# Kernel tuning notes

Measured on AMD Instinct MI355X. Metric: run time of the kernel, lower is better.

## Reference

```python
import jax, jax.numpy as jnp
import numpy as np

N, K, CIN, HID, COUT, E, MH = 8192, 200, 512, 256, 40, 5, 64
KG = K // E
EPS = 1e-5


def setup_inputs() -> dict:
    key = jax.random.key(0)
    ks = jax.random.split(key, 20)
    inp = {
        "X": jax.random.normal(ks[0], (N, CIN), jnp.float32),
        "La": jax.random.uniform(ks[1], (K,), jnp.float32),
        "U": jax.random.normal(ks[2], (N, K), jnp.float32),
        # 5 EigenExperts, each mlp = Linear(1,64) -> ReLU -> Linear(64,64) -> ReLU -> Linear(64,1)
        "eW1": jax.random.normal(ks[3], (E, MH), jnp.float32) * 0.5,
        "eb1": jax.random.normal(ks[4], (E, MH), jnp.float32) * 0.1,
        "eW2": jax.random.normal(ks[5], (E, MH, MH), jnp.float32) * (1.0 / np.sqrt(MH)),
        "eb2": jax.random.normal(ks[6], (E, MH), jnp.float32) * 0.1,
        "eW3": jax.random.normal(ks[7], (E, MH), jnp.float32) * (1.0 / np.sqrt(MH)),
        "eb3": jax.random.normal(ks[8], (E,), jnp.float32) * 0.1,
        # gate: Linear(5,5) -> ReLU -> Linear(5,5) -> Softmax
        "gW1": jax.random.normal(ks[9], (E, E), jnp.float32) * 0.4,
        "gb1": jax.random.normal(ks[10], (E,), jnp.float32) * 0.1,
        "gW2": jax.random.normal(ks[11], (E, E), jnp.float32) * 0.4,
        "gb2": jax.random.normal(ks[12], (E,), jnp.float32) * 0.1,
        # W: Linear(in_channels, hidden_dim)
        "Ww": jax.random.normal(ks[13], (CIN, HID), jnp.float32) * (1.0 / np.sqrt(CIN)),
        "Wb": jax.random.normal(ks[14], (HID,), jnp.float32) * 0.1,
        # BatchNorm1d(hidden_dim), training-mode batch stats
        "bn_gamma": jnp.ones((HID,), jnp.float32),
        "bn_beta": jnp.zeros((HID,), jnp.float32),
        # MLP: Linear(hidden_dim, out_channels)
        "Mw": jax.random.normal(ks[15], (HID, COUT), jnp.float32) * (1.0 / np.sqrt(HID)),
        "Mb": jax.random.normal(ks[16], (COUT,), jnp.float32) * 0.1,
    }
    return inp


def reference(X, La, U, eW1, eb1, eW2, eb2, eW3, eb3, gW1, gb1, gW2, gb2, Ww, Wb, bn_gamma, bn_beta, Mw, Mb):
    n, k = U.shape
    e = eW1.shape[0]
    kg = k // e
    # group eigenvector columns: U[:, i*kg:(i+1)*kg] for expert i -> [n, e, kg]
    Ue = U.reshape(n, e, kg)
    # EigenExpert tiny MLP applied elementwise over entries of each column, then mean over nodes
    h1 = jax.nn.relu(jnp.einsum('nek,eh->nekh', Ue, eW1) + eb1[None, :, None, :])
    h2 = jax.nn.relu(jnp.einsum('nekh,ehg->nekg', h1, eW2) + eb2[None, :, None, :])
    v = jnp.einsum('nekh,eh->nek', h2, eW3) + eb3[None, :, None]
    V = v.mean(axis=0)                      # [e, kg] importance per eigenvector
    # gate on per-group mean eigenvalue
    stats = La.reshape(e, kg).mean(axis=1)  # [e]
    g = jax.nn.relu(stats @ gW1 + gb1) @ gW2 + gb2
    g = jax.nn.softmax(g, axis=-1)          # [e]
    # sum_i g_i * U_i diag(V_i) U_i^T == (U * s) @ U^T with per-column scale s
    s = (g[:, None] * V).reshape(k)         # [k]
    A = (U * s[None, :]) @ U.T              # [n, n]
    out = A @ X                             # [n, cin]
    hidden = out @ Ww + Wb                  # [n, hid]
    mu = hidden.mean(axis=0)
    var = hidden.var(axis=0)                # biased, as torch BN uses for normalization
    h = (hidden - mu) * jax.lax.rsqrt(var + EPS) * bn_gamma + bn_beta
    h = jax.nn.relu(h)                      # dropout is identity (eval)
    logits = h @ Mw + Mb
    return jax.nn.log_softmax(logits, axis=1), hidden
```

## Files before the change

kernel.cpp:

```cpp
#include <hip/hip_runtime.h>
#include <hip/hip_bf16.h>

#define N_    8192
#define K_    200
#define CIN_  512
#define HID_  256
#define COUT_ 40
#define E_    5
#define MH_   64
#define KG_   40
#define EPS_  1e-5f

#define WS_VSUM  0
#define WS_BNSUM 256
#define WS_T     768
#define WS_S     103168
#define WS_G     103424

#define KSPLIT_ 16

typedef __bf16 bf16x8 __attribute__((ext_vector_type(8)));
typedef float  f32x16 __attribute__((ext_vector_type(16)));

__device__ __forceinline__ uint packbf(float a, float b) {
    union { __bf16 h[2]; uint u; } p;
    p.h[0] = (__bf16)a; p.h[1] = (__bf16)b;
    return p.u;
}

union UB { uint4 q; bf16x8 v; };

__global__ __launch_bounds__(256) void k_expert(
    const float* __restrict__ U,
    const float* __restrict__ eW1, const float* __restrict__ eb1,
    const float* __restrict__ eW2, const float* __restrict__ eb2,
    const float* __restrict__ eW3, const float* __restrict__ eb3,
    float* __restrict__ Vsum)
{
    const int e   = blockIdx.x;
    const int tid = threadIdx.x;
    const int w   = tid >> 6;
    const int l   = tid & 63;
    const int lo  = l & 31;
    const int hi  = l >> 5;

    __shared__ uint  spk[4][8][64][4];
    __shared__ float sW1[MH_], sb1[MH_], sb2s[MH_], sW3s[MH_];
    __shared__ float colsum[KG_];

    if (tid < MH_) {
        sW1[tid]  = eW1[e*MH_ + tid];
        sb1[tid]  = eb1[e*MH_ + tid];
        sb2s[tid] = eb2[e*MH_ + tid];
        sW3s[tid] = eW3[e*MH_ + tid];
    }
    if (tid < KG_) colsum[tid] = 0.f;
    const float b3 = eb3[e];

    bf16x8 fa[2][4];
    {
        const float* W2e = eW2 + e*MH_*MH_;
        #pragma unroll
        for (int mt = 0; mt < 2; ++mt) {
            const int grow = mt*32 + lo;
            #pragma unroll
            for (int t = 0; t < 4; ++t) {
                const int k0 = 16*t + 8*hi;
                union { uint u[4]; bf16x8 v; } fb;
                #pragma unroll
                for (int r = 0; r < 4; ++r) {
                    const float x0 = W2e[(k0+2*r  )*MH_ + grow];
                    const float x1 = W2e[(k0+2*r+1)*MH_ + grow];
                    fb.u[r] = packbf(x0, x1);
                }
                fa[mt][t] = fb.v;
            }
        }
    }
    __syncthreads();

    for (int it = 0; it < 4; ++it) {
        const int tile  = (blockIdx.y*16 + it*4 + w);
        const int elem0 = tile * 64;
        const int idx   = elem0 + l;
        const int n     = idx / KG_;
        const int kg    = idx - n*KG_;
        const float u   = U[n*K_ + e*KG_ + kg];

        #pragma unroll
        for (int q = 0; q < 8; ++q) {
            uint wr[4];
            #pragma unroll
            for (int j = 0; j < 4; ++j) {
                const int h = 8*q + 2*j;
                const float a = fmaxf(fmaf(u, sW1[h],   sb1[h]),   0.f);
                const float b = fmaxf(fmaf(u, sW1[h+1], sb1[h+1]), 0.f);
                wr[j] = packbf(a, b);
            }
            *reinterpret_cast<uint4*>(&spk[w][q][l][0]) =
                make_uint4(wr[0], wr[1], wr[2], wr[3]);
        }
        asm volatile("s_waitcnt lgkmcnt(0)" ::: "memory");

        f32x16 acc00 = {0}; f32x16 acc10 = {0};
        f32x16 acc01 = {0}; f32x16 acc11 = {0};
        #pragma unroll
        for (int t = 0; t < 4; ++t) {
            UB b0, b1;
            b0.q = *reinterpret_cast<const uint4*>(&spk[w][2*t+hi][lo   ][0]);
            b1.q = *reinterpret_cast<const uint4*>(&spk[w][2*t+hi][32+lo][0]);
            acc00 = __builtin_amdgcn_mfma_f32_32x32x16_bf16(fa[0][t], b0.v, acc00, 0, 0, 0);
            acc10 = __builtin_amdgcn_mfma_f32_32x32x16_bf16(fa[1][t], b0.v, acc10, 0, 0, 0);
            acc01 = __builtin_amdgcn_mfma_f32_32x32x16_bf16(fa[0][t], b1.v, acc01, 0, 0, 0);
            acc11 = __builtin_amdgcn_mfma_f32_32x32x16_bf16(fa[1][t], b1.v, acc11, 0, 0, 0);
        }

        float vs0 = 0.f, vs1 = 0.f;
        #pragma unroll
        for (int r = 0; r < 16; ++r) {
            const int gb  = (r & 3) + 8*(r >> 2) + 4*hi;
            const float b2a = sb2s[gb],      w3a = sW3s[gb];
            const float b2b = sb2s[32 + gb], w3b = sW3s[32 + gb];
            vs0 += fmaxf(acc00[r] + b2a, 0.f)*w3a + fmaxf(acc10[r] + b2b, 0.f)*w3b;
            vs1 += fmaxf(acc01[r] + b2a, 0.f)*w3a + fmaxf(acc11[r] + b2b, 0.f)*w3b;
        }
        vs0 += __shfl_xor(vs0, 32);
        vs1 += __shfl_xor(vs1, 32);

        const float myv    = (hi ? vs1 : vs0) + b3;
        const int   myelem = (hi ? 32 : 0) + lo;
        const int   mykg   = (elem0 + myelem) % KG_;
        atomicAdd(&colsum[mykg], myv);
    }

    __syncthreads();
    if (tid < KG_) atomicAdd(&Vsum[e*KG_ + tid], colsum[tid]);
}

__global__ void k_gate(
    const float* __restrict__ La,
    const float* __restrict__ gW1, const float* __restrict__ gb1,
    const float* __restrict__ gW2, const float* __restrict__ gb2,
    const float* __restrict__ Vsum, float* __restrict__ s)
{
    __shared__ float sg[E_];
    const int tid = threadIdx.x;
    if (tid == 0) {
        float stats[E_], g1[E_], g2[E_];
        for (int e = 0; e < E_; ++e) {
            float acc = 0.f;
            for (int k = 0; k < KG_; ++k) acc += La[e*KG_ + k];
            stats[e] = acc * (1.0f/KG_);
        }
        for (int j = 0; j < E_; ++j) {
            float acc = gb1[j];
            for (int i = 0; i < E_; ++i) acc += stats[i]*gW1[i*E_ + j];
            g1[j] = fmaxf(acc, 0.f);
        }
        float m = -1e30f;
        for (int j = 0; j < E_; ++j) {
            float acc = gb2[j];
            for (int i = 0; i < E_; ++i) acc += g1[i]*gW2[i*E_ + j];
            g2[j] = acc;
            m = fmaxf(m, acc);
        }
        float ssum = 0.f;
        for (int j = 0; j < E_; ++j) { g2[j] = expf(g2[j]-m); ssum += g2[j]; }
        for (int j = 0; j < E_; ++j) sg[j] = g2[j] / ssum;
    }
    __syncthreads();
    if (tid < K_) s[tid] = sg[tid / KG_] * Vsum[tid] * (1.0f/N_);
}

__global__ __launch_bounds__(256) void k_utx(
    const float* __restrict__ U, const float* __restrict__ X,
    float* __restrict__ P)
{
    const int c0    = blockIdx.x * 32;
    const int ks    = blockIdx.y;
    const int r0    = ks * 512;
    const int mhalf = blockIdx.z;
    const int tid = threadIdx.x;
    const int w   = tid >> 6;
    const int l   = tid & 63;
    const int lo  = l & 31;
    const int hi  = l >> 5;

    __shared__ uint spkX[256][32];

    for (int j = tid; j < 2048; j += 256) {
        const int rp = j >> 3, c4 = j & 7;
        const float4 a = *reinterpret_cast<const float4*>(&X[(r0+2*rp  )*CIN_ + c0 + 4*c4]);
        const float4 b = *reinterpret_cast<const float4*>(&X[(r0+2*rp+1)*CIN_ + c0 + 4*c4]);
        uint4 pk;
        pk.x = packbf(a.x, b.x); pk.y = packbf(a.y, b.y);
        pk.z = packbf(a.z, b.z); pk.w = packbf(a.w, b.w);
        *reinterpret_cast<uint4*>(&spkX[rp][4*c4]) = pk;
    }
    __syncthreads();

    const int mt   = mhalf*4 + w;
    const int colc = min(32*mt + lo, K_ - 1);

    f32x16 acc = {0};
    #pragma unroll 2
    for (int it = 0; it < 16; ++it) {
        const int rb = r0 + 32*it;
        #pragma unroll
        for (int t = 0; t < 2; ++t) {
            const int kr = rb + 16*t + 8*hi;
            union { uint u[4]; bf16x8 v; } ax;
            #pragma unroll
            for (int j2 = 0; j2 < 4; ++j2) {
                const float f0 = U[(kr + 2*j2    )*K_ + colc];
                const float f1 = U[(kr + 2*j2 + 1)*K_ + colc];
                ax.u[j2] = packbf(f0, f1);
            }
            UB bx;
            const int rpb = 16*it + 8*t + 4*hi;
            bx.q.x = spkX[rpb+0][lo];
            bx.q.y = spkX[rpb+1][lo];
            bx.q.z = spkX[rpb+2][lo];
            bx.q.w = spkX[rpb+3][lo];
            acc = __builtin_amdgcn_mfma_f32_32x32x16_bf16(ax.v, bx.v, acc, 0, 0, 0);
        }
    }

    #pragma unroll
    for (int r = 0; r < 16; ++r) {
        const int mm = 32*mt + (r & 3) + 8*(r >> 2) + 4*hi;
        if (mm < K_)
            P[(ks*K_ + mm)*CIN_ + c0 + lo] = acc[r];
    }
}

__global__ __launch_bounds__(256) void k_red(
    const float* __restrict__ P, float* __restrict__ T)
{
    const int j = blockIdx.x*256 + threadIdx.x;
    float4 s = {0.f, 0.f, 0.f, 0.f};
    for (int ks = 0; ks < KSPLIT_; ++ks) {
        const float4 v = *reinterpret_cast<const float4*>(&P[ks*K_*CIN_ + j*4]);
        s.x += v.x; s.y += v.y; s.z += v.z; s.w += v.w;
    }
    *reinterpret_cast<float4*>(&T[j*4]) = s;
}

__global__ __launch_bounds__(256) void k_g(
    const float* __restrict__ T, const float* __restrict__ Ww,
    float* __restrict__ G)
{
    const int k0  = blockIdx.x * 4;
    const int c   = threadIdx.x;
    __shared__ float4 sT4[4][128];

    for (int j = threadIdx.x; j < 512; j += 256) {
        const int r = j >> 7, c4 = j & 127;
        sT4[r][c4] = reinterpret_cast<const float4*>(T)[(k0+r)*128 + c4];
    }
    __syncthreads();

    float a0 = 0.f, a1 = 0.f, a2 = 0.f, a3 = 0.f;
    for (int ci4 = 0; ci4 < 128; ++ci4) {
        const float w0 = Ww[(4*ci4+0)*HID_ + c];
        const float w1 = Ww[(4*ci4+1)*HID_ + c];
        const float w2 = Ww[(4*ci4+2)*HID_ + c];
        const float w3 = Ww[(4*ci4+3)*HID_ + c];
        float4 t;
        t = sT4[0][ci4]; a0 += t.x*w0 + t.y*w1 + t.z*w2 + t.w*w3;
        t = sT4[1][ci4]; a1 += t.x*w0 + t.y*w1 + t.z*w2 + t.w*w3;
        t = sT4[2][ci4]; a2 += t.x*w0 + t.y*w1 + t.z*w2 + t.w*w3;
        t = sT4[3][ci4]; a3 += t.x*w0 + t.y*w1 + t.z*w2 + t.w*w3;
    }
    G[(k0+0)*HID_ + c] = a0;
    G[(k0+1)*HID_ + c] = a1;
    G[(k0+2)*HID_ + c] = a2;
    G[(k0+3)*HID_ + c] = a3;
}

__global__ __launch_bounds__(256) void k_hidden(
    const float* __restrict__ U, const float* __restrict__ s,
    const float* __restrict__ G, const float* __restrict__ Wb,
    float* __restrict__ hid)
{
    const int c0  = blockIdx.x * 64;
    const int n0  = blockIdx.y * 128;
    const int tid = threadIdx.x;
    const int w   = tid >> 6;
    const int l   = tid & 63;
    const int lo  = l & 31;
    const int hi  = l >> 5;

    __shared__ uint  spkA[104][128];
    __shared__ uint  spkB[104][64];
    __shared__ float ss[K_];

    if (tid < K_) ss[tid] = s[tid];
    __syncthreads();

    for (int j = tid; j < 128*26; j += 256) {
        const int m = j & 127, g = j >> 7;
        uint4 pk = make_uint4(0u, 0u, 0u, 0u);
        if (g < 25) {
            const float4 a = *reinterpret_cast<const float4*>(&U[(n0+m)*K_ + 8*g]);
            const float4 b = *reinterpret_cast<const float4*>(&U[(n0+m)*K_ + 8*g + 4]);
            pk.x = packbf(a.x*ss[8*g+0], a.y*ss[8*g+1]);
            pk.y = packbf(a.z*ss[8*g+2], a.w*ss[8*g+3]);
            pk.z = packbf(b.x*ss[8*g+4], b.y*ss[8*g+5]);
            pk.w = packbf(b.z*ss[8*g+6], b.w*ss[8*g+7]);
        }
        spkA[4*g+0][m] = pk.x;
        spkA[4*g+1][m] = pk.y;
        spkA[4*g+2][m] = pk.z;
        spkA[4*g+3][m] = pk.w;
    }
    for (int j = tid; j < 64*26; j += 256) {
        const int c = j & 63, g = j >> 6;
        uint4 pk = make_uint4(0u, 0u, 0u, 0u);
        if (g < 25) {
            const float v0 = G[(8*g+0)*HID_ + c0+c], v1 = G[(8*g+1)*HID_ + c0+c];
            const float v2 = G[(8*g+2)*HID_ + c0+c], v3 = G[(8*g+3)*HID_ + c0+c];
            const float v4 = G[(8*g+4)*HID_ + c0+c], v5 = G[(8*g+5)*HID_ + c0+c];
            const float v6 = G[(8*g+6)*HID_ + c0+c], v7 = G[(8*g+7)*HID_ + c0+c];
            pk.x = packbf(v0, v1); pk.y = packbf(v2, v3);
            pk.z = packbf(v4, v5); pk.w = packbf(v6, v7);
        }
        spkB[4*g+0][c] = pk.x;
        spkB[4*g+1][c] = pk.y;
        spkB[4*g+2][c] = pk.z;
        spkB[4*g+3][c] = pk.w;
    }
    __syncthreads();

    f32x16 acc0 = {0}, acc1 = {0};
    #pragma unroll
    for (int t = 0; t < 13; ++t) {
        const int kp = 8*t + 4*hi;
        union { uint u[4]; bf16x8 v; } fa;
        fa.u[0] = spkA[kp+0][32*w + lo];
        fa.u[1] = spkA[kp+1][32*w + lo];
        fa.u[2] = spkA[kp+2][32*w + lo];
        fa.u[3] = spkA[kp+3][32*w + lo];
        UB b0, b1;
        b0.q.x = spkB[kp+0][lo];      b0.q.y = spkB[kp+1][lo];
        b0.q.z = spkB[kp+2][lo];      b0.q.w = spkB[kp+3][lo];
        b1.q.x = spkB[kp+0][32 + lo]; b1.q.y = spkB[kp+1][32 + lo];
        b1.q.z = spkB[kp+2][32 + lo]; b1.q.w = spkB[kp+3][32 + lo];
        acc0 = __builtin_amdgcn_mfma_f32_32x32x16_bf16(fa.v, b0.v, acc0, 0, 0, 0);
        acc1 = __builtin_amdgcn_mfma_f32_32x32x16_bf16(fa.v, b1.v, acc1, 0, 0, 0);
    }

    const float wb0 = Wb[c0 + lo], wb1 = Wb[c0 + 32 + lo];
    #pragma unroll
    for (int r = 0; r < 16; ++r) {
        const int row = 32*w + (r & 3) + 8*(r >> 2) + 4*hi;
        hid[(n0+row)*HID_ + c0 + lo]      = acc0[r] + wb0;
        hid[(n0+row)*HID_ + c0 + 32 + lo] = acc1[r] + wb1;
    }
}

__global__ __launch_bounds__(256) void k_bnstat(
    const float* __restrict__ hid, float* __restrict__ bnsum)
{
    const int c  = threadIdx.x;
    const int n0 = blockIdx.x * 32;
    float sm = 0.f, sq = 0.f;
    for (int r = 0; r < 32; ++r) {
        const float v = hid[(n0+r)*HID_ + c];
        sm += v; sq += v*v;
    }
    atomicAdd(&bnsum[c], sm);
    atomicAdd(&bnsum[HID_ + c], sq);
}

__global__ __launch_bounds__(256) void k_logits(
    const float* __restrict__ hid, const float* __restrict__ bnsum,
    const float* __restrict__ gamma, const float* __restrict__ beta,
    const float* __restrict__ Mw, const float* __restrict__ Mb,
    float* __restrict__ outls)
{
    __shared__ float sc[HID_], sh[HID_], sMb[COUT_];
    __shared__ float sMw[HID_][COUT_];
    __shared__ float sPart[8][32][41];

    const int tid = threadIdx.x;
    const int r   = tid & 31;
    const int sl  = tid >> 5;

    {
        const float sm = bnsum[tid], sq = bnsum[HID_+tid];
        const float mu  = sm * (1.0f/N_);
        const float var = sq * (1.0f/N_) - mu*mu;
        const float a   = gamma[tid] * rsqrtf(var + EPS_);
        sc[tid] = a;
        sh[tid] = beta[tid] - mu*a;
    }
    for (int j = tid; j < HID_*COUT_/4; j += 256)
        reinterpret_cast<float4*>(&sMw[0][0])[j] = reinterpret_cast<const float4*>(Mw)[j];
    if (tid < COUT_) sMb[tid] = Mb[tid];
    __syncthreads();

    const int n  = blockIdx.x*32 + r;
    const int cb = sl * 32;
    float acc[COUT_];
    #pragma unroll
    for (int j = 0; j < COUT_; ++j) acc[j] = 0.f;

    const float4* hrow = reinterpret_cast<const float4*>(&hid[n*HID_ + cb]);
    #pragma unroll
    for (int c4 = 0; c4 < 8; ++c4) {
        const float4 h4 = hrow[c4];
        const float hv[4] = {h4.x, h4.y, h4.z, h4.w};
        #pragma unroll
        for (int q = 0; q < 4; ++q) {
            const int c = cb + 4*c4 + q;
            const float hn = fmaxf(hv[q]*sc[c] + sh[c], 0.f);
            #pragma unroll
            for (int j0 = 0; j0 < COUT_; j0 += 4) {
                const float4 wv = *reinterpret_cast<const float4*>(&sMw[c][j0]);
                acc[j0+0] += hn*wv.x; acc[j0+1] += hn*wv.y;
                acc[j0+2] += hn*wv.z; acc[j0+3] += hn*wv.w;
            }
        }
    }
    #pragma unroll
    for (int j = 0; j < COUT_; ++j) sPart[sl][r][j] = acc[j];
    __syncthreads();

    if (tid < 32) {
        const int n2 = blockIdx.x*32 + tid;
        float a2[COUT_];
        #pragma unroll
        for (int j = 0; j < COUT_; ++j) {
            float sum = sMb[j];
            #pragma unroll
            for (int s2 = 0; s2 < 8; ++s2) sum += sPart[s2][tid][j];
            a2[j] = sum;
        }
        float m = -1e30f;
        #pragma unroll
        for (int j = 0; j < COUT_; ++j) m = fmaxf(m, a2[j]);
        float ssum = 0.f;
        #pragma unroll
        for (int j = 0; j < COUT_; ++j) ssum += expf(a2[j] - m);
        const float lse = m + logf(ssum);
        #pragma unroll
        for (int j = 0; j < COUT_; ++j)
            outls[n2*COUT_ + j] = a2[j] - lse;
    }
}

extern "C" void kernel_launch(void* const* d_in, const int* in_sizes, int n_in,
                              void* d_out, int out_size, void* d_ws, size_t ws_size,
                              hipStream_t stream)
{
    const float* X        = (const float*)d_in[0];
    const float* La       = (const float*)d_in[1];
    const float* U        = (const float*)d_in[2];
    const float* eW1      = (const float*)d_in[3];
    const float* eb1      = (const float*)d_in[4];
    const float* eW2      = (const float*)d_in[5];
    const float* eb2      = (const float*)d_in[6];
    const float* eW3      = (const float*)d_in[7];
    const float* eb3      = (const float*)d_in[8];
    const float* gW1      = (const float*)d_in[9];
    const float* gb1      = (const float*)d_in[10];
    const float* gW2      = (const float*)d_in[11];
    const float* gb2      = (const float*)d_in[12];
    const float* Ww       = (const float*)d_in[13];
    const float* Wb       = (const float*)d_in[14];
    const float* bn_gamma = (const float*)d_in[15];
    const float* bn_beta  = (const float*)d_in[16];
    const float* Mw       = (const float*)d_in[17];
    const float* Mb       = (const float*)d_in[18];

    float* out   = (float*)d_out;
    float* ws    = (float*)d_ws;
    float* Vsum  = ws + WS_VSUM;
    float* bnsum = ws + WS_BNSUM;
    float* T     = ws + WS_T;
    float* s     = ws + WS_S;
    float* G     = ws + WS_G;

    float* outls = out;
    float* hid   = out + N_*COUT_;
    float* P     = out;

    hipMemsetAsync(ws, 0, (size_t)768 * sizeof(float), stream);

    k_utx   <<<dim3(16, KSPLIT_, 2), 256, 0, stream>>>(U, X, P);
    k_expert<<<dim3(E_, 320),        256, 0, stream>>>(U, eW1, eb1, eW2, eb2, eW3, eb3, Vsum);
    k_gate  <<<1,   256, 0, stream>>>(La, gW1, gb1, gW2, gb2, Vsum, s);
    k_red   <<<100, 256, 0, stream>>>(P, T);
    k_g     <<<50,  256, 0, stream>>>(T, Ww, G);
    k_hidden<<<dim3(4, 64), 256, 0, stream>>>(U, s, G, Wb, hid);
    k_bnstat<<<256, 256, 0, stream>>>(hid, bnsum);
    k_logits<<<256, 256, 0, stream>>>(hid, bnsum, bn_gamma, bn_beta, Mw, Mb, outls);
}
```

Before: 245.1 us.

## Replace split-K partials with atomic accumulation and build expert MFMA operands in registers

k_utx now splits the U^T X reduction into 64 slices of 128 rows and accumulates directly into T with atomicAdd. This removes the partial-sum buffer and the separate k_red reduction kernel, and X is loaded straight into registers instead of being staged in shared memory. In k_expert, the first-layer activations are computed per lane from shuffled u values and packed into MFMA B operands directly, which drops the shared-memory staging buffer. The costs are many fp32 atomics on a 200x512 output, a larger memset, uncoalesced strided X loads, and a non-deterministic summation order.

Measured after the change: 235.8 us. 3.8% less time.

```diff
diff --git a/kernel.cpp b/kernel.cpp
--- a/kernel.cpp
+++ b/kernel.cpp
@@ -17,8 +17,6 @@
 #define WS_S     103168
 #define WS_G     103424
 
-#define KSPLIT_ 16
-
 typedef __bf16 bf16x8 __attribute__((ext_vector_type(8)));
 typedef float  f32x16 __attribute__((ext_vector_type(16)));
 
@@ -44,7 +42,6 @@
     const int lo  = l & 31;
     const int hi  = l >> 5;
 
-    __shared__ uint  spk[4][8][64][4];
     __shared__ float sW1[MH_], sb1[MH_], sb2s[MH_], sW3s[MH_];
     __shared__ float colsum[KG_];
 
@@ -87,28 +84,30 @@
         const int kg    = idx - n*KG_;
         const float u   = U[n*K_ + e*KG_ + kg];
 
-        #pragma unroll
-        for (int q = 0; q < 8; ++q) {
-            uint wr[4];
-            #pragma unroll
-            for (int j = 0; j < 4; ++j) {
-                const int h = 8*q + 2*j;
-                const float a = fmaxf(fmaf(u, sW1[h],   sb1[h]),   0.f);
-                const float b = fmaxf(fmaf(u, sW1[h+1], sb1[h+1]), 0.f);
-                wr[j] = packbf(a, b);
-            }
-            *reinterpret_cast<uint4*>(&spk[w][q][l][0]) =
-                make_uint4(wr[0], wr[1], wr[2], wr[3]);
-        }
-        asm volatile("s_waitcnt lgkmcnt(0)" ::: "memory");
+        const float ucol0 = __shfl(u, lo);
+        const float ucol1 = __shfl(u, 32 + lo);
 
         f32x16 acc00 = {0}; f32x16 acc10 = {0};
         f32x16 acc01 = {0}; f32x16 acc11 = {0};
         #pragma unroll
         for (int t = 0; t < 4; ++t) {
-            UB b0, b1;
-            b0.q = *reinterpret_cast<const uint4*>(&spk[w][2*t+hi][lo   ][0]);
-            b1.q = *reinterpret_cast<const uint4*>(&spk[w][2*t+hi][32+lo][0]);
+            const int k0 = 16*t + 8*hi;
+            float2 w1p[4], b1p[4];
+            #pragma unroll
+            for (int r = 0; r < 4; ++r) {
+                w1p[r] = *reinterpret_cast<const float2*>(&sW1[k0 + 2*r]);
+                b1p[r] = *reinterpret_cast<const float2*>(&sb1[k0 + 2*r]);
+            }
+            union { uint u[4]; bf16x8 v; } b0, b1;
+            #pragma unroll
+            for (int r = 0; r < 4; ++r) {
+                const float pa = fmaxf(fmaf(ucol0, w1p[r].x, b1p[r].x), 0.f);
+                const float pb = fmaxf(fmaf(ucol0, w1p[r].y, b1p[r].y), 0.f);
+                b0.u[r] = packbf(pa, pb);
+                const float qa = fmaxf(fmaf(ucol1, w1p[r].x, b1p[r].x), 0.f);
+                const float qb = fmaxf(fmaf(ucol1, w1p[r].y, b1p[r].y), 0.f);
+                b1.u[r] = packbf(qa, qb);
+            }
             acc00 = __builtin_amdgcn_mfma_f32_32x32x16_bf16(fa[0][t], b0.v, acc00, 0, 0, 0);
             acc10 = __builtin_amdgcn_mfma_f32_32x32x16_bf16(fa[1][t], b0.v, acc10, 0, 0, 0);
             acc01 = __builtin_amdgcn_mfma_f32_32x32x16_bf16(fa[0][t], b1.v, acc01, 0, 0, 0);
@@ -174,11 +173,10 @@
 
 __global__ __launch_bounds__(256) void k_utx(
     const float* __restrict__ U, const float* __restrict__ X,
-    float* __restrict__ P)
+    float* __restrict__ T)
 {
     const int c0    = blockIdx.x * 32;
-    const int ks    = blockIdx.y;
-    const int r0    = ks * 512;
+    const int r0    = blockIdx.y * 128;
     const int mhalf = blockIdx.z;
     const int tid = threadIdx.x;
     const int w   = tid >> 6;
@@ -186,64 +184,33 @@
     const int lo  = l & 31;
     const int hi  = l >> 5;
 
-    __shared__ uint spkX[256][32];
-
-    for (int j = tid; j < 2048; j += 256) {
-        const int rp = j >> 3, c4 = j & 7;
-        const float4 a = *reinterpret_cast<const float4*>(&X[(r0+2*rp  )*CIN_ + c0 + 4*c4]);
-        const float4 b = *reinterpret_cast<const float4*>(&X[(r0+2*rp+1)*CIN_ + c0 + 4*c4]);
-        uint4 pk;
-        pk.x = packbf(a.x, b.x); pk.y = packbf(a.y, b.y);
-        pk.z = packbf(a.z, b.z); pk.w = packbf(a.w, b.w);
-        *reinterpret_cast<uint4*>(&spkX[rp][4*c4]) = pk;
-    }
-    __syncthreads();
-
     const int mt   = mhalf*4 + w;
     const int colc = min(32*mt + lo, K_ - 1);
+    const int xcol = c0 + lo;
 
     f32x16 acc = {0};
-    #pragma unroll 2
-    for (int it = 0; it < 16; ++it) {
-        const int rb = r0 + 32*it;
-        #pragma unroll
-        for (int t = 0; t < 2; ++t) {
-            const int kr = rb + 16*t + 8*hi;
-            union { uint u[4]; bf16x8 v; } ax;
-            #pragma unroll
-            for (int j2 = 0; j2 < 4; ++j2) {
-                const float f0 = U[(kr + 2*j2    )*K_ + colc];
-                const float f1 = U[(kr + 2*j2 + 1)*K_ + colc];
-                ax.u[j2] = packbf(f0, f1);
-            }
-            UB bx;
-            const int rpb = 16*it + 8*t + 4*hi;
-            bx.q.x = spkX[rpb+0][lo];
-            bx.q.y = spkX[rpb+1][lo];
-            bx.q.z = spkX[rpb+2][lo];
-            bx.q.w = spkX[rpb+3][lo];
-            acc = __builtin_amdgcn_mfma_f32_32x32x16_bf16(ax.v, bx.v, acc, 0, 0, 0);
-        }
+    #pragma unroll
+    for (int s = 0; s < 8; ++s) {
+        const int kr = r0 + 16*s + 8*hi;
+        union { uint u[4]; bf16x8 v; } ax, bx;
+        #pragma unroll
+        for (int j2 = 0; j2 < 4; ++j2) {
+            const float ua = U[(kr + 2*j2    )*K_ + colc];
+            const float ub = U[(kr + 2*j2 + 1)*K_ + colc];
+            ax.u[j2] = packbf(ua, ub);
+            const float xa = X[(kr + 2*j2    )*CIN_ + xcol];
+            const float xb = X[(kr + 2*j2 + 1)*CIN_ + xcol];
+            bx.u[j2] = packbf(xa, xb);
+        }
+        acc = __builtin_amdgcn_mfma_f32_32x32x16_bf16(ax.v, bx.v, acc, 0, 0, 0);
     }
 
     #pragma unroll
     for (int r = 0; r < 16; ++r) {
         const int mm = 32*mt + (r & 3) + 8*(r >> 2) + 4*hi;
         if (mm < K_)
-            P[(ks*K_ + mm)*CIN_ + c0 + lo] = acc[r];
-    }
-}
-
-__global__ __launch_bounds__(256) void k_red(
-    const float* __restrict__ P, float* __restrict__ T)
-{
-    const int j = blockIdx.x*256 + threadIdx.x;
-    float4 s = {0.f, 0.f, 0.f, 0.f};
-    for (int ks = 0; ks < KSPLIT_; ++ks) {
-        const float4 v = *reinterpret_cast<const float4*>(&P[ks*K_*CIN_ + j*4]);
-        s.x += v.x; s.y += v.y; s.z += v.z; s.w += v.w;
-    }
-    *reinterpret_cast<float4*>(&T[j*4]) = s;
+            atomicAdd(&T[mm*CIN_ + c0 + lo], acc[r]);
+    }
 }
 
 __global__ __launch_bounds__(256) void k_g(
@@ -484,14 +451,12 @@
 
     float* outls = out;
     float* hid   = out + N_*COUT_;
-    float* P     = out;
-
-    hipMemsetAsync(ws, 0, (size_t)768 * sizeof(float), stream);
-
-    k_utx   <<<dim3(16, KSPLIT_, 2), 256, 0, stream>>>(U, X, P);
-    k_expert<<<dim3(E_, 320),        256, 0, stream>>>(U, eW1, eb1, eW2, eb2, eW3, eb3, Vsum);
+
+    hipMemsetAsync(ws, 0, (size_t)(WS_T + K_*CIN_) * sizeof(float), stream);
+
+    k_utx   <<<dim3(16, 64, 2), 256, 0, stream>>>(U, X, T);
+    k_expert<<<dim3(E_, 320),   256, 0, stream>>>(U, eW1, eb1, eW2, eb2, eW3, eb3, Vsum);
     k_gate  <<<1,   256, 0, stream>>>(La, gW1, gb1, gW2, gb2, Vsum, s);
-    k_red   <<<100, 256, 0, stream>>>(P, T);
     k_g     <<<50,  256, 0, stream>>>(T, Ww, G);
     k_hidden<<<dim3(4, 64), 256, 0, stream>>>(U, s, G, Wb, hid);
     k_bnstat<<<256, 256, 0, stream>>>(hid, bnsum);
```
